# Kernel tuning notes

Hardware: AMD Instinct MI355X
Metric: run time of the kernel (lower is better)

The kernel has to match this reference:

```python
import jax, jax.numpy as jnp
import numpy as np

B, C, N, V, H = 8, 256, 1024, 12, 4
D = C // H  # 64
BN_EPS = 1e-5
NEG = 1e10


def _vconv(x, W, b, g, bt, m4):
    """VointConv block: 1x1 conv + BN(batch stats) + relu, with reset_voint_mask
    applied after every sublayer (as in the torch loop).
    x: [B, Cin, N, V], W: [Cout, Cin], m4: [B, 1, N, V] float mask."""
    y = (jnp.einsum('oc,bcnv->bonv', W, x) + b[None, :, None, None]) * m4
    mu = jnp.mean(y, axis=(0, 2, 3), keepdims=True)
    var = jnp.var(y, axis=(0, 2, 3), keepdims=True)
    y = ((y - mu) * jax.lax.rsqrt(var + BN_EPS) * g[None, :, None, None]
         + bt[None, :, None, None]) * m4
    return jax.nn.relu(y) * m4


def setup_inputs() -> dict:
    key = jax.random.key(0)
    ks = jax.random.split(key, 20)
    inp = {}
    inp['voints_feats'] = jax.random.normal(ks[0], (B, C, N, V), jnp.float32)
    inp['voints_mask'] = (jax.random.uniform(ks[1], (B, N, V)) > 0.3).astype(jnp.float32)
    w = lambda k, shp: (jax.random.normal(k, shp, jnp.float32) * 0.05)
    # embed_layers[0]: VointConv([C, C/heads])
    inp['We'] = w(ks[2], (D, C)); inp['be'] = w(ks[3], (D,))
    inp['ge'] = 1.0 + 0.1 * jax.random.normal(ks[4], (D,), jnp.float32)
    inp['bne'] = 0.1 * jax.random.normal(ks[5], (D,), jnp.float32)
    # embed_atten_layers[0]: VointConv([C/heads, 3*C])
    inp['Wa'] = w(ks[6], (3 * C, D)); inp['ba'] = w(ks[7], (3 * C,))
    inp['ga'] = 1.0 + 0.1 * jax.random.normal(ks[8], (3 * C,), jnp.float32)
    inp['bna'] = 0.1 * jax.random.normal(ks[9], (3 * C,), jnp.float32)
    # to_out[0]: VointConv([C, C])
    inp['Wo'] = w(ks[10], (C, C)); inp['bo'] = w(ks[11], (C,))
    inp['go'] = 1.0 + 0.1 * jax.random.normal(ks[12], (C,), jnp.float32)
    inp['bno'] = 0.1 * jax.random.normal(ks[13], (C,), jnp.float32)
    # feedforward[0]: VointConv([C, C])
    inp['Wf'] = w(ks[14], (C, C)); inp['bf'] = w(ks[15], (C,))
    inp['gf'] = 1.0 + 0.1 * jax.random.normal(ks[16], (C,), jnp.float32)
    inp['bnf'] = 0.1 * jax.random.normal(ks[17], (C,), jnp.float32)
    return inp


def reference(voints_feats, voints_mask, We, be, ge, bne, Wa, ba, ga, bna,
              Wo, bo, go, bno, Wf, bf, gf, bnf):
    mask = voints_mask                      # [B, N, V] float
    m4 = mask[:, None, :, :]                # [B, 1, N, V]
    # embedding to per-head dim, then joint QKV projection
    emb = _vconv(voints_feats, We, be, ge, bne, m4)      # [B, D, N, V]
    qkv = _vconv(emb, Wa, ba, ga, bna, m4)               # [B, 3C, N, V]
    k, q, v = jnp.split(qkv, 3, axis=1)                  # torch.chunk order: k, q, v
    resh = lambda t: t.reshape(B, H, D, N, V)            # 'b (h d) n v -> b h d n v'
    q, k, v = resh(q), resh(k), resh(v)
    scale = float(C) ** (-0.5)
    dots = jnp.einsum('bhdnv,bhdnj->bhnvj', q, k) * scale  # [B,H,N,V,V]
    empty = jnp.sum(mask, axis=-1) == 0                  # [B, N]
    dots = jnp.where(empty[:, None, :, None, None], 0.0, dots)
    # vointsoftmax: bias broadcasts over query dim v (mask[...,None] -> [B,1,N,V,1])
    qbias = jnp.where(mask[:, None, :, :, None] > 0, 0.0, -NEG)
    attn = jax.nn.softmax(dots + qbias, axis=-1) * mask[:, None, :, :, None]
    # faithful to source: 'b h n v j, b h d n v -> b h n v d' (j summed over attn only)
    out = jnp.einsum('bhnvj,bhdnv->bhnvd', attn, v)      # [B,H,N,V,D]
    out = out.transpose(0, 1, 4, 2, 3).reshape(B, C, N, V)  # 'b h n v d -> b (h d) n v'
    out = jnp.where(empty[:, None, :, None], 0.0, out)
    out = _vconv(out, Wo, bo, go, bno, m4)
    x = voints_feats + out
    x = x + _vconv(x, Wf, bf, gf, bnf, m4)
    return x
```

## Files before the change

### kernel.cpp

```cpp
#include <hip/hip_runtime.h>
#include <hip/hip_bf16.h>

typedef __attribute__((ext_vector_type(8))) __bf16 bf16x8;
typedef __attribute__((ext_vector_type(4))) float floatx4;
typedef __attribute__((ext_vector_type(8))) unsigned short ushort8;

namespace {
constexpr int kC  = 256;
constexpr int kNV = 1024 * 12;
constexpr int kP  = 8 * kNV;
constexpr float kEps = 1e-5f;

constexpr size_t OFF_PART   = 2048;
constexpr size_t OFF_WB     = 2048 + 16384;
constexpr size_t OFF_XT     = OFF_WB + 81920;
constexpr size_t OFF_Y1     = OFF_XT + (size_t)kP * 256 / 2;
constexpr size_t OFF_Y2     = OFF_Y1 + (size_t)kP * 64 / 2;
constexpr size_t OFF_Y3     = OFF_Y2 + (size_t)kP * 256 / 2;
}

__device__ __forceinline__ unsigned short f2bf(float f) {
    unsigned int u = __builtin_bit_cast(unsigned int, f);
    u += 0x7FFFu + ((u >> 16) & 1u);
    return (unsigned short)(u >> 16);
}
__device__ __forceinline__ float bf2f(unsigned short h) {
    unsigned int u = ((unsigned int)h) << 16;
    return __builtin_bit_cast(float, u);
}
__device__ __forceinline__ unsigned int f2bf2(float lo, float hi) {
    unsigned int r;
    asm("v_cvt_pk_bf16_f32 %0, %1, %2" : "=v"(r) : "v"(lo), "v"(hi));
    return r;
}

__global__ void convw_kernel(const float* __restrict__ We, const float* __restrict__ Wa,
                             const float* __restrict__ Wo, const float* __restrict__ Wf,
                             unsigned short* __restrict__ dst)
{
    const int f = (blockIdx.x * 256 + threadIdx.x) * 4;
    const float* src; int off, M, K, base;
    if (f < 16384)      { src = We;            off = f;         M = 64;  K = 256; base = 0; }
    else if (f < 32768) { src = Wa + 512 * 64; off = f - 16384; M = 256; K = 64;  base = 16384; }
    else if (f < 98304) { src = Wo;            off = f - 32768; M = 256; K = 256; base = 32768; }
    else                { src = Wf;            off = f - 98304; M = 256; K = 256; base = 98304; }
    const int m = off / K, k = off - m * K;
    const float4 v = *(const float4*)&src[off];
    ushort4 o; o.x = f2bf(v.x); o.y = f2bf(v.y); o.z = f2bf(v.z); o.w = f2bf(v.w);
    *(ushort4*)&dst[base + (k >> 5) * (M * 32) + m * 32 + (k & 31)] = o;
}

__global__ __launch_bounds__(256) void transpose_kernel(
    const float* __restrict__ x, unsigned short* __restrict__ xT)
{
    __shared__ float T[64][65];
    const int p0 = blockIdx.x * 64;
    const int c0 = blockIdx.y * 64;
    const int b  = p0 / kNV;
    const int q0 = p0 - b * kNV;
    const int t  = threadIdx.x;

    const int cl = t >> 2;
    const int pq = (t & 3) * 16;
    const float* src = &x[(size_t)(b * kC + c0 + cl) * kNV + q0 + pq];
    #pragma unroll
    for (int i = 0; i < 4; ++i) {
        const float4 v = *(const float4*)&src[i * 4];
        T[cl][pq + i * 4 + 0] = v.x;
        T[cl][pq + i * 4 + 1] = v.y;
        T[cl][pq + i * 4 + 2] = v.z;
        T[cl][pq + i * 4 + 3] = v.w;
    }
    __syncthreads();
    const int pr = t >> 2;
    const int cb = (t & 3) * 16;
    #pragma unroll
    for (int i = 0; i < 2; ++i) {
        ushort8 o;
        #pragma unroll
        for (int j = 0; j < 8; ++j) o[j] = f2bf(T[cb + i * 8 + j][pr]);
        *(ushort8*)&xT[(size_t)(p0 + pr) * 256 + c0 + cb + i * 8] = o;
    }
}

template<int MODE>
__device__ __forceinline__ ushort8 xform(ushort8 y8, ushort8 x8, float mp,
                                         const float* __restrict__ actA,
                                         const float* __restrict__ actB, int kk)
{
    if constexpr (MODE == 0) {
        return y8;
    } else {
        const float4 a0 = *(const float4*)&actA[kk];
        const float4 a1 = *(const float4*)&actA[kk + 4];
        const float4 b0 = *(const float4*)&actB[kk];
        const float4 b1 = *(const float4*)&actB[kk + 4];
        const float aa[8] = {a0.x, a0.y, a0.z, a0.w, a1.x, a1.y, a1.z, a1.w};
        const float bb[8] = {b0.x, b0.y, b0.z, b0.w, b1.x, b1.y, b1.z, b1.w};
        float v[8];
        #pragma unroll
        for (int j = 0; j < 8; ++j) {
            float t = mp * fmaxf(fmaf(aa[j], bf2f(y8[j]), bb[j]), 0.f);
            if constexpr (MODE == 2) t += bf2f(x8[j]);
            v[j] = t;
        }
        uint4 u;
        u.x = f2bf2(v[0], v[1]); u.y = f2bf2(v[2], v[3]);
        u.z = f2bf2(v[4], v[5]); u.w = f2bf2(v[6], v[7]);
        return __builtin_bit_cast(ushort8, u);
    }
}

template<int BM, int MTOT, int K, int MODE, int SIBS, int MINW>
__global__ __launch_bounds__(256, MINW) void gemm_kernel(
    const unsigned short* __restrict__ Apk, const float* __restrict__ bias,
    const unsigned short* __restrict__ Yprev, const unsigned short* __restrict__ XT,
    const float* __restrict__ mask,
    const float* __restrict__ pPrev, const float* __restrict__ gPrev,
    const float* __restrict__ btPrev,
    unsigned short* __restrict__ Yout, float* __restrict__ partial, int slabsPerBlock)
{
    constexpr int LD = 264;
    constexpr int NT = K / 32;
    constexpr int FM = BM / 64;
    constexpr int FP = 2;
    constexpr int CH = K / 64;
    __shared__ unsigned short Bs[2][32 * LD];
    __shared__ float ActA[256];
    __shared__ float ActB[256];

    const int tid  = threadIdx.x;
    const int w    = tid >> 6, lane = tid & 63, quad = lane >> 4, lt = lane & 15;
    const int mBase = w * 16 * FM;

    int groupId, sib;
    if constexpr (SIBS > 1) {
        const int x = blockIdx.x & 7;
        const int s = blockIdx.x >> 3;
        const int perX = (int)(gridDim.x >> 3) / SIBS;
        sib = s % SIBS;
        groupId = x * perX + s / SIBS;
    } else {
        groupId = blockIdx.x; sib = 0;
    }
    const int chOff = sib * BM;
    const int slab0 = groupId * slabsPerBlock;

    if constexpr (MODE != 0) {
        if (tid < K) {
            float s = 0.f, s2 = 0.f;
            #pragma unroll
            for (int k = 0; k < 8; ++k) {
                s  += pPrev[k * 512 + tid];
                s2 += pPrev[k * 512 + 256 + tid];
            }
            const float mu  = s * (1.f / kP);
            const float var = s2 * (1.f / kP) - mu * mu;
            const float A   = rsqrtf(var + kEps) * gPrev[tid];
            ActA[tid] = A;
            ActB[tid] = fmaf(-mu, A, btPrev[tid]);
        }
        __syncthreads();
    }

    ushort8 Areg[NT][FM];
    #pragma unroll
    for (int t = 0; t < NT; ++t)
        #pragma unroll
        for (int fm = 0; fm < FM; ++fm)
            Areg[t][fm] = *(const ushort8*)&Apk[(size_t)(t * MTOT + chOff + mBase + fm * 16 + lt) * 32 + quad * 8];

    float biR[FM][4];
    #pragma unroll
    for (int fm = 0; fm < FM; ++fm) {
        const float4 b4 = *(const float4*)&bias[chOff + mBase + fm * 16 + quad * 4];
        biR[fm][0] = b4.x; biR[fm][1] = b4.y; biR[fm][2] = b4.z; biR[fm][3] = b4.w;
    }

    float aS[FM][4], aQ[FM][4];
    #pragma unroll
    for (int fm = 0; fm < FM; ++fm)
        #pragma unroll
        for (int i = 0; i < 4; ++i) { aS[fm][i] = 0.f; aQ[fm][i] = 0.f; }

    const int spb = slabsPerBlock;

    {
        const int pBase = slab0 * 32;
        #pragma unroll
        for (int i = 0; i < CH; ++i) {
            const int c = tid + i * 256;
            const int p = c / (K / 8);
            const int kq = (c % (K / 8)) * 8;
            const ushort8 y8 = *(const ushort8*)&Yprev[(size_t)(pBase + p) * K + kq];
            ushort8 o;
            if constexpr (MODE == 0) o = y8;
            else {
                ushort8 x8{};
                if constexpr (MODE == 2) x8 = *(const ushort8*)&XT[(size_t)(pBase + p) * K + kq];
                o = xform<MODE>(y8, x8, mask[pBase + p], ActA, ActB, kq);
            }
            *(ushort8*)&Bs[0][p * LD + kq] = o;
        }
    }
    __syncthreads();

    for (int s = 0; s < spb; ++s) {
        const int pBase = (slab0 + s) * 32;
        const bool hasNext = (s + 1 < spb);

        ushort8 py[CH];
        ushort8 px[(MODE == 2) ? CH : 1];
        if (hasNext) {
            const int pN = (slab0 + s + 1) * 32;
            #pragma unroll
            for (int i = 0; i < CH; ++i) {
                const int c = tid + i * 256;
                const int p = c / (K / 8);
                const int kq = (c % (K / 8)) * 8;
                py[i] = *(const ushort8*)&Yprev[(size_t)(pN + p) * K + kq];
                if constexpr (MODE == 2)
                    px[i] = *(const ushort8*)&XT[(size_t)(pN + p) * K + kq];
            }
        }

        floatx4 acc[FM][FP];
        #pragma unroll
        for (int fm = 0; fm < FM; ++fm)
            #pragma unroll
            for (int fp = 0; fp < FP; ++fp) acc[fm][fp] = (floatx4)0.f;

        const unsigned short* bs = &Bs[s & 1][0];
        #pragma unroll
        for (int t = 0; t < NT; ++t) {
            bf16x8 bF[FP];
            #pragma unroll
            for (int fp = 0; fp < FP; ++fp)
                bF[fp] = *(const bf16x8*)&bs[(fp * 16 + lt) * LD + t * 32 + quad * 8];
            #pragma unroll
            for (int fm = 0; fm < FM; ++fm) {
                const bf16x8 aF = __builtin_bit_cast(bf16x8, Areg[t][fm]);
                #pragma unroll
                for (int fp = 0; fp < FP; ++fp)
                    acc[fm][fp] = __builtin_amdgcn_mfma_f32_16x16x32_bf16(aF, bF[fp], acc[fm][fp], 0, 0, 0);
            }
        }

        float mpv[FP];
        #pragma unroll
        for (int fp = 0; fp < FP; ++fp) mpv[fp] = mask[pBase + fp * 16 + lt];

        #pragma unroll
        for (int fm = 0; fm < FM; ++fm) {
            #pragma unroll
            for (int fp = 0; fp < FP; ++fp) {
                const int pG = pBase + fp * 16 + lt;
                float vv[4];
                #pragma unroll
                for (int i = 0; i < 4; ++i) {
                    const float v = (acc[fm][fp][i] + biR[fm][i]) * mpv[fp];
                    vv[i] = v; aS[fm][i] += v; aQ[fm][i] += v * v;
                }
                uint2 o; o.x = f2bf2(vv[0], vv[1]); o.y = f2bf2(vv[2], vv[3]);
                *(uint2*)&Yout[(size_t)pG * MTOT + chOff + mBase + fm * 16 + quad * 4] = o;
            }
        }

        if (hasNext) {
            const int pN = (slab0 + s + 1) * 32;
            unsigned short* bn = &Bs[(s + 1) & 1][0];
            #pragma unroll
            for (int i = 0; i < CH; ++i) {
                const int c = tid + i * 256;
                const int p = c / (K / 8);
                const int kq = (c % (K / 8)) * 8;
                ushort8 o;
                if constexpr (MODE == 0) o = py[i];
                else {
                    ushort8 x8{};
                    if constexpr (MODE == 2) x8 = px[i];
                    o = xform<MODE>(py[i], x8, mask[pN + p], ActA, ActB, kq);
                }
                *(ushort8*)&bn[p * LD + kq] = o;
            }
        }
        __syncthreads();
    }

    #pragma unroll
    for (int fm = 0; fm < FM; ++fm)
        #pragma unroll
        for (int i = 0; i < 4; ++i) {
            #pragma unroll
            for (int off = 1; off < 16; off <<= 1) {
                aS[fm][i] += __shfl_xor(aS[fm][i], off);
                aQ[fm][i] += __shfl_xor(aQ[fm][i], off);
            }
        }
    if (lt == 0) {
        float* pb = partial + (size_t)(blockIdx.x & 7) * 512;
        #pragma unroll
        for (int fm = 0; fm < FM; ++fm)
            #pragma unroll
            for (int i = 0; i < 4; ++i) {
                const int ch = chOff + mBase + fm * 16 + quad * 4 + i;
                atomicAdd(&pb[ch], aS[fm][i]);
                atomicAdd(&pb[256 + ch], aQ[fm][i]);
            }
    }
}

__global__ __launch_bounds__(256) void final_kernel(
    const unsigned short* __restrict__ xT, const unsigned short* __restrict__ y3,
    const unsigned short* __restrict__ y4,
    const float* __restrict__ p3, const float* __restrict__ g3, const float* __restrict__ bt3,
    const float* __restrict__ p4, const float* __restrict__ g4, const float* __restrict__ bt4,
    const float* __restrict__ mask, float* __restrict__ out)
{
    constexpr int TL = 264;
    __shared__ unsigned short TX[32 * TL];
    __shared__ unsigned short T4[32 * TL];
    __shared__ float PA3[256], PB3[256], PA4[256], PB4[256];
    const int p0 = blockIdx.x * 32;
    const int b  = p0 / kNV;
    const int q0 = p0 - b * kNV;

    {
        const int m = threadIdx.x;
        float s3 = 0.f, q3 = 0.f, s4 = 0.f, q4 = 0.f;
        #pragma unroll
        for (int k = 0; k < 8; ++k) {
            s3 += p3[k * 512 + m]; q3 += p3[k * 512 + 256 + m];
            s4 += p4[k * 512 + m]; q4 += p4[k * 512 + 256 + m];
        }
        const float mu3 = s3 * (1.f / kP);
        const float A3  = rsqrtf(q3 * (1.f / kP) - mu3 * mu3 + kEps) * g3[m];
        PA3[m] = A3; PB3[m] = fmaf(-mu3, A3, bt3[m]);
        const float mu4 = s4 * (1.f / kP);
        const float A4  = rsqrtf(q4 * (1.f / kP) - mu4 * mu4 + kEps) * g4[m];
        PA4[m] = A4; PB4[m] = fmaf(-mu4, A4, bt4[m]);
    }
    __syncthreads();

    #pragma unroll
    for (int i = 0; i < 4; ++i) {
        const int idx = threadIdx.x + i * 256;
        const int p = idx >> 5, c0 = (idx & 31) * 8;
        const ushort8 x8  = *(const ushort8*)&xT[(size_t)(p0 + p) * 256 + c0];
        const ushort8 y38 = *(const ushort8*)&y3[(size_t)(p0 + p) * 256 + c0];
        const ushort8 y48 = *(const ushort8*)&y4[(size_t)(p0 + p) * 256 + c0];
        const float mp = mask[p0 + p];
        ushort8 o;
        #pragma unroll
        for (int j = 0; j < 8; ++j) {
            const int c = c0 + j;
            const float x1 = bf2f(x8[j]) + mp * fmaxf(fmaf(PA3[c], bf2f(y38[j]), PB3[c]), 0.f);
            o[j] = f2bf(x1);
        }
        *(ushort8*)&TX[p * TL + c0] = o;
        *(ushort8*)&T4[p * TL + c0] = y48;
    }
    __syncthreads();

    const int qv = (threadIdx.x & 15) * 2;
    const int cb = threadIdx.x >> 4;
    const float m0v = mask[p0 + qv], m1v = mask[p0 + qv + 1];
    #pragma unroll
    for (int j = 0; j < 16; ++j) {
        const int c = cb + j * 16;
        const float a4 = PA4[c], b4 = PB4[c];
        const size_t ro = (size_t)(b * kC + c) * kNV + q0 + qv;
        float2 o;
        o.x = bf2f(TX[qv * TL + c])       + m0v * fmaxf(fmaf(a4, bf2f(T4[qv * TL + c]), b4), 0.f);
        o.y = bf2f(TX[(qv + 1) * TL + c]) + m1v * fmaxf(fmaf(a4, bf2f(T4[(qv + 1) * TL + c]), b4), 0.f);
        *(float2*)&out[ro] = o;
    }
}

extern "C" void kernel_launch(void* const* d_in, const int* in_sizes, int n_in,
                              void* d_out, int out_size, void* d_ws, size_t ws_size,
                              hipStream_t stream)
{
    const float* x    = (const float*)d_in[0];
    const float* mask = (const float*)d_in[1];
    const float* We   = (const float*)d_in[2];
    const float* be   = (const float*)d_in[3];
    const float* ge   = (const float*)d_in[4];
    const float* bne  = (const float*)d_in[5];
    const float* Wa   = (const float*)d_in[6];
    const float* ba   = (const float*)d_in[7];
    const float* ga   = (const float*)d_in[8];
    const float* bna  = (const float*)d_in[9];
    const float* Wo   = (const float*)d_in[10];
    const float* bo   = (const float*)d_in[11];
    const float* go   = (const float*)d_in[12];
    const float* bno  = (const float*)d_in[13];
    const float* Wf   = (const float*)d_in[14];
    const float* bf   = (const float*)d_in[15];
    const float* gf   = (const float*)d_in[16];
    const float* bnf  = (const float*)d_in[17];
    float* out = (float*)d_out;
    float* ws  = (float*)d_ws;

    float* part = ws + OFF_PART;
    unsigned short* Wb = (unsigned short*)(ws + OFF_WB);
    unsigned short* xT = (unsigned short*)(ws + OFF_XT);
    unsigned short* y1 = (unsigned short*)(ws + OFF_Y1);
    unsigned short* y2 = (unsigned short*)(ws + OFF_Y2);
    unsigned short* y3 = (unsigned short*)(ws + OFF_Y3);

    hipMemsetAsync(part, 0, 16384 * sizeof(float), stream);
    convw_kernel<<<160, 256, 0, stream>>>(We, Wa, Wo, Wf, Wb);
    transpose_kernel<<<dim3(kP / 64, 4), 256, 0, stream>>>(x, xT);

    const dim3 blk(256);

    gemm_kernel<64, 64, 256, 0, 1, 4><<<1024, blk, 0, stream>>>(
        Wb, be, xT, nullptr, mask, nullptr, nullptr, nullptr, y1, part, 3);

    gemm_kernel<128, 256, 64, 1, 2, 4><<<1024, blk, 0, stream>>>(
        Wb + 16384, ba + 512, y1, nullptr, mask, part, ge, bne, y2, part + 4096, 6);

    gemm_kernel<128, 256, 256, 1, 2, 3><<<768, blk, 0, stream>>>(
        Wb + 32768, bo, y2, nullptr, mask, part + 4096, ga + 512, bna + 512, y3, part + 8192, 8);

    gemm_kernel<128, 256, 256, 2, 2, 3><<<768, blk, 0, stream>>>(
        Wb + 98304, bf, y3, xT, mask, part + 8192, go, bno, y2, part + 12288, 8);

    final_kernel<<<kP / 32, blk, 0, stream>>>(
        xT, y3, y2, part + 8192, go, bno, part + 12288, gf, bnf, mask, out);
}
```

Baseline: 389.2 us.

## Triple-buffer GEMM B tiles with two-slab-ahead register prefetch and retune launches

The GEMM main loop moves from double to triple LDS buffering. Global loads of Y, X and the mask are now issued two slabs ahead into alternating register sets, and the LDS store for the next slab happens before the epilogue, with a single lightweight barrier per step. The goal is to hide global memory latency behind the MFMA work. The launch configurations also change: the first GEMM uses fewer, larger blocks, and the two 256x256 GEMMs switch to BM=64 with four sibling blocks and 16 slabs each. In exchange this raises register and LDS pressure, and the loop unrolled by two assumes spb is even.

```diff
diff --git a/kernel.cpp b/kernel.cpp
--- a/kernel.cpp
+++ b/kernel.cpp
@@ -32,6 +32,12 @@
     unsigned int r;
     asm("v_cvt_pk_bf16_f32 %0, %1, %2" : "=v"(r) : "v"(lo), "v"(hi));
     return r;
+}
+
+__device__ __forceinline__ void phase_barrier() {
+    asm volatile("s_waitcnt lgkmcnt(0)" ::: "memory");
+    __builtin_amdgcn_s_barrier();
+    asm volatile("" ::: "memory");
 }
 
 __global__ void convw_kernel(const float* __restrict__ We, const float* __restrict__ Wa,
@@ -120,12 +126,13 @@
     const float* __restrict__ btPrev,
     unsigned short* __restrict__ Yout, float* __restrict__ partial, int slabsPerBlock)
 {
-    constexpr int LD = 264;
+    constexpr int LD = K + 8;
     constexpr int NT = K / 32;
     constexpr int FM = BM / 64;
     constexpr int FP = 2;
     constexpr int CH = K / 64;
-    __shared__ unsigned short Bs[2][32 * LD];
+    constexpr int XH = (MODE == 2) ? CH : 1;
+    __shared__ unsigned short Bs[3][32 * LD];
     __shared__ float ActA[256];
     __shared__ float ActB[256];
 
@@ -144,7 +151,8 @@
         groupId = blockIdx.x; sib = 0;
     }
     const int chOff = sib * BM;
-    const int slab0 = groupId * slabsPerBlock;
+    const int spb   = slabsPerBlock;
+    const int slab0 = groupId * spb;
 
     if constexpr (MODE != 0) {
         if (tid < K) {
@@ -183,7 +191,10 @@
         #pragma unroll
         for (int i = 0; i < 4; ++i) { aS[fm][i] = 0.f; aQ[fm][i] = 0.f; }
 
-    const int spb = slabsPerBlock;
+    ushort8 pyA[CH], pyB[CH];
+    ushort8 pxA[XH], pxB[XH];
+    float   mxA[CH], mxB[CH];
+    float   meA[FP], meB[FP];
 
     {
         const int pBase = slab0 * 32;
@@ -202,25 +213,39 @@
             }
             *(ushort8*)&Bs[0][p * LD + kq] = o;
         }
-    }
-    __syncthreads();
-
-    for (int s = 0; s < spb; ++s) {
-        const int pBase = (slab0 + s) * 32;
-        const bool hasNext = (s + 1 < spb);
-
-        ushort8 py[CH];
-        ushort8 px[(MODE == 2) ? CH : 1];
-        if (hasNext) {
-            const int pN = (slab0 + s + 1) * 32;
+        #pragma unroll
+        for (int fp = 0; fp < FP; ++fp) meA[fp] = mask[pBase + fp * 16 + lt];
+        const int pN = (slab0 + 1) * 32;
+        #pragma unroll
+        for (int i = 0; i < CH; ++i) {
+            const int c = tid + i * 256;
+            const int p = c / (K / 8);
+            const int kq = (c % (K / 8)) * 8;
+            pyA[i] = *(const ushort8*)&Yprev[(size_t)(pN + p) * K + kq];
+            if constexpr (MODE == 2) pxA[i] = *(const ushort8*)&XT[(size_t)(pN + p) * K + kq];
+            if constexpr (MODE != 0) mxA[i] = mask[pN + p];
+        }
+    }
+    phase_barrier();
+
+    auto stepf = [&](int s, int cur,
+                     ushort8 (&uy)[CH], ushort8 (&ux)[XH], float (&umx)[CH], float (&ume)[FP],
+                     ushort8 (&fy)[CH], ushort8 (&fx)[XH], float (&fmx)[CH], float (&fme)[FP]) {
+        if (s + 1 < spb) {
+            const int pE = (slab0 + s + 1) * 32;
+            #pragma unroll
+            for (int fp = 0; fp < FP; ++fp) fme[fp] = mask[pE + fp * 16 + lt];
+        }
+        if (s + 2 < spb) {
+            const int pN = (slab0 + s + 2) * 32;
             #pragma unroll
             for (int i = 0; i < CH; ++i) {
                 const int c = tid + i * 256;
                 const int p = c / (K / 8);
                 const int kq = (c % (K / 8)) * 8;
-                py[i] = *(const ushort8*)&Yprev[(size_t)(pN + p) * K + kq];
-                if constexpr (MODE == 2)
-                    px[i] = *(const ushort8*)&XT[(size_t)(pN + p) * K + kq];
+                fy[i] = *(const ushort8*)&Yprev[(size_t)(pN + p) * K + kq];
+                if constexpr (MODE == 2) fx[i] = *(const ushort8*)&XT[(size_t)(pN + p) * K + kq];
+                if constexpr (MODE != 0) fmx[i] = mask[pN + p];
             }
         }
 
@@ -230,7 +255,7 @@
             #pragma unroll
             for (int fp = 0; fp < FP; ++fp) acc[fm][fp] = (floatx4)0.f;
 
-        const unsigned short* bs = &Bs[s & 1][0];
+        const unsigned short* bs = &Bs[cur][0];
         #pragma unroll
         for (int t = 0; t < NT; ++t) {
             bf16x8 bF[FP];
@@ -246,10 +271,26 @@
             }
         }
 
-        float mpv[FP];
-        #pragma unroll
-        for (int fp = 0; fp < FP; ++fp) mpv[fp] = mask[pBase + fp * 16 + lt];
-
+        if (s + 1 < spb) {
+            const int nb = (cur == 2) ? 0 : cur + 1;
+            unsigned short* bn = &Bs[nb][0];
+            #pragma unroll
+            for (int i = 0; i < CH; ++i) {
+                const int c = tid + i * 256;
+                const int p = c / (K / 8);
+                const int kq = (c % (K / 8)) * 8;
+                ushort8 o;
+                if constexpr (MODE == 0) o = uy[i];
+                else {
+                    ushort8 x8{};
+                    if constexpr (MODE == 2) x8 = ux[i];
+                    o = xform<MODE>(uy[i], x8, umx[i], ActA, ActB, kq);
+                }
+                *(ushort8*)&bn[p * LD + kq] = o;
+            }
+        }
+
+        const int pBase = (slab0 + s) * 32;
         #pragma unroll
         for (int fm = 0; fm < FM; ++fm) {
             #pragma unroll
@@ -258,7 +299,7 @@
                 float vv[4];
                 #pragma unroll
                 for (int i = 0; i < 4; ++i) {
-                    const float v = (acc[fm][fp][i] + biR[fm][i]) * mpv[fp];
+                    const float v = (acc[fm][fp][i] + biR[fm][i]) * ume[fp];
                     vv[i] = v; aS[fm][i] += v; aQ[fm][i] += v * v;
                 }
                 uint2 o; o.x = f2bf2(vv[0], vv[1]); o.y = f2bf2(vv[2], vv[3]);
@@ -266,25 +307,15 @@
             }
         }
 
-        if (hasNext) {
-            const int pN = (slab0 + s + 1) * 32;
-            unsigned short* bn = &Bs[(s + 1) & 1][0];
-            #pragma unroll
-            for (int i = 0; i < CH; ++i) {
-                const int c = tid + i * 256;
-                const int p = c / (K / 8);
-                const int kq = (c % (K / 8)) * 8;
-                ushort8 o;
-                if constexpr (MODE == 0) o = py[i];
-                else {
-                    ushort8 x8{};
-                    if constexpr (MODE == 2) x8 = px[i];
-                    o = xform<MODE>(py[i], x8, mask[pN + p], ActA, ActB, kq);
-                }
-                *(ushort8*)&bn[p * LD + kq] = o;
-            }
-        }
-        __syncthreads();
+        phase_barrier();
+    };
+
+    int cur = 0;
+    for (int s = 0; s < spb; s += 2) {
+        stepf(s,     cur, pyA, pxA, mxA, meA, pyB, pxB, mxB, meB);
+        cur = (cur == 2) ? 0 : cur + 1;
+        stepf(s + 1, cur, pyB, pxB, mxB, meB, pyA, pxA, mxA, meA);
+        cur = (cur == 2) ? 0 : cur + 1;
     }
 
     #pragma unroll
@@ -415,17 +446,17 @@
 
     const dim3 blk(256);
 
-    gemm_kernel<64, 64, 256, 0, 1, 4><<<1024, blk, 0, stream>>>(
-        Wb, be, xT, nullptr, mask, nullptr, nullptr, nullptr, y1, part, 3);
+    gemm_kernel<64, 64, 256, 0, 1, 3><<<768, blk, 0, stream>>>(
+        Wb, be, xT, nullptr, mask, nullptr, nullptr, nullptr, y1, part, 4);
 
     gemm_kernel<128, 256, 64, 1, 2, 4><<<1024, blk, 0, stream>>>(
         Wb + 16384, ba + 512, y1, nullptr, mask, part, ge, bne, y2, part + 4096, 6);
 
-    gemm_kernel<128, 256, 256, 1, 2, 3><<<768, blk, 0, stream>>>(
-        Wb + 32768, bo, y2, nullptr, mask, part + 4096, ga + 512, bna + 512, y3, part + 8192, 8);
-
-    gemm_kernel<128, 256, 256, 2, 2, 3><<<768, blk, 0, stream>>>(
-        Wb + 98304, bf, y3, xT, mask, part + 8192, go, bno, y2, part + 12288, 8);
+    gemm_kernel<64, 256, 256, 1, 4, 3><<<768, blk, 0, stream>>>(
+        Wb + 32768, bo, y2, nullptr, mask, part + 4096, ga + 512, bna + 512, y3, part + 8192, 16);
+
+    gemm_kernel<64, 256, 256, 2, 4, 3><<<768, blk, 0, stream>>>(
+        Wb + 98304, bf, y3, xT, mask, part + 8192, go, bno, y2, part + 12288, 16);
 
     final_kernel<<<kP / 32, blk, 0, stream>>>(
         xT, y3, y2, part + 8192, go, bno, part + 12288, gf, bnf, mask, out);
```

New measurement: 381.0 us. 1.02x faster.

## Restructure GEMM to one 16-channel slice per wave with configurable waves/slab

Applied to the files above, without the earlier changes.

Each wave now owns a single 16-channel M slice instead of FM slices. Block size (NW waves) and slab width (FP*16 points) become template parameters, so the 128-channel GEMMs run 512-thread blocks and the K=64 GEMM uses 64-point slabs. Mask values are prefetched together with the next slab. The epilogue stores and statistics are moved after the next-slab LDS write, and __syncthreads is replaced by a manual lgkmcnt wait plus s_barrier. This is meant to cut per-thread register pressure and raise occupancy and latency hiding, at the cost of more barriers per block and different grid decompositions.

```diff
diff --git a/kernel.cpp b/kernel.cpp
--- a/kernel.cpp
+++ b/kernel.cpp
@@ -32,6 +32,12 @@
     unsigned int r;
     asm("v_cvt_pk_bf16_f32 %0, %1, %2" : "=v"(r) : "v"(lo), "v"(hi));
     return r;
+}
+
+__device__ __forceinline__ void phase_barrier() {
+    asm volatile("s_waitcnt lgkmcnt(0)" ::: "memory");
+    __builtin_amdgcn_s_barrier();
+    asm volatile("" ::: "memory");
 }
 
 __global__ void convw_kernel(const float* __restrict__ We, const float* __restrict__ Wa,
@@ -111,8 +117,8 @@
     }
 }
 
-template<int BM, int MTOT, int K, int MODE, int SIBS, int MINW>
-__global__ __launch_bounds__(256, MINW) void gemm_kernel(
+template<int BM, int MTOT, int K, int MODE, int SIBS, int NW, int FP, int MINW>
+__global__ __launch_bounds__(NW * 64, MINW) void gemm_kernel(
     const unsigned short* __restrict__ Apk, const float* __restrict__ bias,
     const unsigned short* __restrict__ Yprev, const unsigned short* __restrict__ XT,
     const float* __restrict__ mask,
@@ -120,18 +126,21 @@
     const float* __restrict__ btPrev,
     unsigned short* __restrict__ Yout, float* __restrict__ partial, int slabsPerBlock)
 {
-    constexpr int LD = 264;
+    constexpr int THREADS = NW * 64;
+    constexpr int SLAB = FP * 16;
+    constexpr int LD = K + 8;
     constexpr int NT = K / 32;
-    constexpr int FM = BM / 64;
-    constexpr int FP = 2;
-    constexpr int CH = K / 64;
-    __shared__ unsigned short Bs[2][32 * LD];
+    constexpr int KR = K / 8;
+    constexpr int CH = SLAB * KR / THREADS;
+    constexpr int XH = (MODE == 2) ? CH : 1;
+    static_assert(BM == NW * 16, "one 16-channel slice per wave");
+    __shared__ unsigned short Bs[2][SLAB * LD];
     __shared__ float ActA[256];
     __shared__ float ActB[256];
 
     const int tid  = threadIdx.x;
     const int w    = tid >> 6, lane = tid & 63, quad = lane >> 4, lt = lane & 15;
-    const int mBase = w * 16 * FM;
+    const int mBase = w * 16;
 
     int groupId, sib;
     if constexpr (SIBS > 1) {
@@ -144,7 +153,8 @@
         groupId = blockIdx.x; sib = 0;
     }
     const int chOff = sib * BM;
-    const int slab0 = groupId * slabsPerBlock;
+    const int spb   = slabsPerBlock;
+    const int slab0 = groupId * spb;
 
     if constexpr (MODE != 0) {
         if (tid < K) {
@@ -163,35 +173,28 @@
         __syncthreads();
     }
 
-    ushort8 Areg[NT][FM];
+    ushort8 Areg[NT];
     #pragma unroll
     for (int t = 0; t < NT; ++t)
-        #pragma unroll
-        for (int fm = 0; fm < FM; ++fm)
-            Areg[t][fm] = *(const ushort8*)&Apk[(size_t)(t * MTOT + chOff + mBase + fm * 16 + lt) * 32 + quad * 8];
-
-    float biR[FM][4];
-    #pragma unroll
-    for (int fm = 0; fm < FM; ++fm) {
-        const float4 b4 = *(const float4*)&bias[chOff + mBase + fm * 16 + quad * 4];
-        biR[fm][0] = b4.x; biR[fm][1] = b4.y; biR[fm][2] = b4.z; biR[fm][3] = b4.w;
-    }
-
-    float aS[FM][4], aQ[FM][4];
-    #pragma unroll
-    for (int fm = 0; fm < FM; ++fm)
-        #pragma unroll
-        for (int i = 0; i < 4; ++i) { aS[fm][i] = 0.f; aQ[fm][i] = 0.f; }
-
-    const int spb = slabsPerBlock;
-
+        Areg[t] = *(const ushort8*)&Apk[(size_t)(t * MTOT + chOff + mBase + lt) * 32 + quad * 8];
+
+    float biR[4];
     {
-        const int pBase = slab0 * 32;
+        const float4 b4 = *(const float4*)&bias[chOff + mBase + quad * 4];
+        biR[0] = b4.x; biR[1] = b4.y; biR[2] = b4.z; biR[3] = b4.w;
+    }
+
+    float aS[4], aQ[4];
+    #pragma unroll
+    for (int i = 0; i < 4; ++i) { aS[i] = 0.f; aQ[i] = 0.f; }
+
+    {
+        const int pBase = slab0 * SLAB;
         #pragma unroll
         for (int i = 0; i < CH; ++i) {
-            const int c = tid + i * 256;
-            const int p = c / (K / 8);
-            const int kq = (c % (K / 8)) * 8;
+            const int c = tid + i * THREADS;
+            const int p = c / KR;
+            const int kq = (c % KR) * 8;
             const ushort8 y8 = *(const ushort8*)&Yprev[(size_t)(pBase + p) * K + kq];
             ushort8 o;
             if constexpr (MODE == 0) o = y8;
@@ -203,110 +206,103 @@
             *(ushort8*)&Bs[0][p * LD + kq] = o;
         }
     }
-    __syncthreads();
+    float mCur[FP];
+    #pragma unroll
+    for (int fp = 0; fp < FP; ++fp) mCur[fp] = mask[slab0 * SLAB + fp * 16 + lt];
+    phase_barrier();
 
     for (int s = 0; s < spb; ++s) {
-        const int pBase = (slab0 + s) * 32;
+        const int pBase = (slab0 + s) * SLAB;
         const bool hasNext = (s + 1 < spb);
 
         ushort8 py[CH];
-        ushort8 px[(MODE == 2) ? CH : 1];
+        ushort8 px[XH];
+        float mxN[CH];
+        float mNxt[FP];
         if (hasNext) {
-            const int pN = (slab0 + s + 1) * 32;
+            const int pN = pBase + SLAB;
             #pragma unroll
             for (int i = 0; i < CH; ++i) {
-                const int c = tid + i * 256;
-                const int p = c / (K / 8);
-                const int kq = (c % (K / 8)) * 8;
+                const int c = tid + i * THREADS;
+                const int p = c / KR;
+                const int kq = (c % KR) * 8;
                 py[i] = *(const ushort8*)&Yprev[(size_t)(pN + p) * K + kq];
-                if constexpr (MODE == 2)
-                    px[i] = *(const ushort8*)&XT[(size_t)(pN + p) * K + kq];
-            }
-        }
-
-        floatx4 acc[FM][FP];
-        #pragma unroll
-        for (int fm = 0; fm < FM; ++fm)
-            #pragma unroll
-            for (int fp = 0; fp < FP; ++fp) acc[fm][fp] = (floatx4)0.f;
+                if constexpr (MODE == 2) px[i] = *(const ushort8*)&XT[(size_t)(pN + p) * K + kq];
+                if constexpr (MODE != 0) mxN[i] = mask[pN + c / KR];
+            }
+            #pragma unroll
+            for (int fp = 0; fp < FP; ++fp) mNxt[fp] = mask[pN + fp * 16 + lt];
+        }
+
+        floatx4 acc[FP];
+        #pragma unroll
+        for (int fp = 0; fp < FP; ++fp) acc[fp] = (floatx4)0.f;
 
         const unsigned short* bs = &Bs[s & 1][0];
         #pragma unroll
         for (int t = 0; t < NT; ++t) {
-            bf16x8 bF[FP];
-            #pragma unroll
-            for (int fp = 0; fp < FP; ++fp)
-                bF[fp] = *(const bf16x8*)&bs[(fp * 16 + lt) * LD + t * 32 + quad * 8];
-            #pragma unroll
-            for (int fm = 0; fm < FM; ++fm) {
-                const bf16x8 aF = __builtin_bit_cast(bf16x8, Areg[t][fm]);
-                #pragma unroll
-                for (int fp = 0; fp < FP; ++fp)
-                    acc[fm][fp] = __builtin_amdgcn_mfma_f32_16x16x32_bf16(aF, bF[fp], acc[fm][fp], 0, 0, 0);
-            }
-        }
-
-        float mpv[FP];
-        #pragma unroll
-        for (int fp = 0; fp < FP; ++fp) mpv[fp] = mask[pBase + fp * 16 + lt];
-
-        #pragma unroll
-        for (int fm = 0; fm < FM; ++fm) {
+            const bf16x8 aF = __builtin_bit_cast(bf16x8, Areg[t]);
             #pragma unroll
             for (int fp = 0; fp < FP; ++fp) {
-                const int pG = pBase + fp * 16 + lt;
-                float vv[4];
-                #pragma unroll
-                for (int i = 0; i < 4; ++i) {
-                    const float v = (acc[fm][fp][i] + biR[fm][i]) * mpv[fp];
-                    vv[i] = v; aS[fm][i] += v; aQ[fm][i] += v * v;
-                }
-                uint2 o; o.x = f2bf2(vv[0], vv[1]); o.y = f2bf2(vv[2], vv[3]);
-                *(uint2*)&Yout[(size_t)pG * MTOT + chOff + mBase + fm * 16 + quad * 4] = o;
+                const bf16x8 bF = *(const bf16x8*)&bs[(fp * 16 + lt) * LD + t * 32 + quad * 8];
+                acc[fp] = __builtin_amdgcn_mfma_f32_16x16x32_bf16(aF, bF, acc[fp], 0, 0, 0);
             }
         }
 
         if (hasNext) {
-            const int pN = (slab0 + s + 1) * 32;
             unsigned short* bn = &Bs[(s + 1) & 1][0];
             #pragma unroll
             for (int i = 0; i < CH; ++i) {
-                const int c = tid + i * 256;
-                const int p = c / (K / 8);
-                const int kq = (c % (K / 8)) * 8;
+                const int c = tid + i * THREADS;
+                const int p = c / KR;
+                const int kq = (c % KR) * 8;
                 ushort8 o;
                 if constexpr (MODE == 0) o = py[i];
                 else {
                     ushort8 x8{};
                     if constexpr (MODE == 2) x8 = px[i];
-                    o = xform<MODE>(py[i], x8, mask[pN + p], ActA, ActB, kq);
+                    o = xform<MODE>(py[i], x8, mxN[i], ActA, ActB, kq);
                 }
                 *(ushort8*)&bn[p * LD + kq] = o;
             }
         }
-        __syncthreads();
-    }
-
-    #pragma unroll
-    for (int fm = 0; fm < FM; ++fm)
-        #pragma unroll
-        for (int i = 0; i < 4; ++i) {
-            #pragma unroll
-            for (int off = 1; off < 16; off <<= 1) {
-                aS[fm][i] += __shfl_xor(aS[fm][i], off);
-                aQ[fm][i] += __shfl_xor(aQ[fm][i], off);
-            }
-        }
+
+        #pragma unroll
+        for (int fp = 0; fp < FP; ++fp) {
+            const int pG = pBase + fp * 16 + lt;
+            float vv[4];
+            #pragma unroll
+            for (int i = 0; i < 4; ++i) {
+                const float v = (acc[fp][i] + biR[i]) * mCur[fp];
+                vv[i] = v; aS[i] += v; aQ[i] += v * v;
+            }
+            uint2 o; o.x = f2bf2(vv[0], vv[1]); o.y = f2bf2(vv[2], vv[3]);
+            *(uint2*)&Yout[(size_t)pG * MTOT + chOff + mBase + quad * 4] = o;
+        }
+        if (hasNext) {
+            #pragma unroll
+            for (int fp = 0; fp < FP; ++fp) mCur[fp] = mNxt[fp];
+        }
+
+        phase_barrier();
+    }
+
+    #pragma unroll
+    for (int i = 0; i < 4; ++i) {
+        #pragma unroll
+        for (int off = 1; off < 16; off <<= 1) {
+            aS[i] += __shfl_xor(aS[i], off);
+            aQ[i] += __shfl_xor(aQ[i], off);
+        }
+    }
     if (lt == 0) {
         float* pb = partial + (size_t)(blockIdx.x & 7) * 512;
         #pragma unroll
-        for (int fm = 0; fm < FM; ++fm)
-            #pragma unroll
-            for (int i = 0; i < 4; ++i) {
-                const int ch = chOff + mBase + fm * 16 + quad * 4 + i;
-                atomicAdd(&pb[ch], aS[fm][i]);
-                atomicAdd(&pb[256 + ch], aQ[fm][i]);
-            }
+        for (int i = 0; i < 4; ++i) {
+            const int ch = chOff + mBase + quad * 4 + i;
+            atomicAdd(&pb[ch], aS[i]);
+            atomicAdd(&pb[256 + ch], aQ[i]);
+        }
     }
 }
 
@@ -413,20 +409,18 @@
     convw_kernel<<<160, 256, 0, stream>>>(We, Wa, Wo, Wf, Wb);
     transpose_kernel<<<dim3(kP / 64, 4), 256, 0, stream>>>(x, xT);
 
-    const dim3 blk(256);
-
-    gemm_kernel<64, 64, 256, 0, 1, 4><<<1024, blk, 0, stream>>>(
-        Wb, be, xT, nullptr, mask, nullptr, nullptr, nullptr, y1, part, 3);
-
-    gemm_kernel<128, 256, 64, 1, 2, 4><<<1024, blk, 0, stream>>>(
-        Wb + 16384, ba + 512, y1, nullptr, mask, part, ge, bne, y2, part + 4096, 6);
-
-    gemm_kernel<128, 256, 256, 1, 2, 3><<<768, blk, 0, stream>>>(
+    gemm_kernel<64, 64, 256, 0, 1, 4, 2, 3><<<768, 256, 0, stream>>>(
+        Wb, be, xT, nullptr, mask, nullptr, nullptr, nullptr, y1, part, 4);
+
+    gemm_kernel<128, 256, 64, 1, 2, 8, 4, 4><<<768, 512, 0, stream>>>(
+        Wb + 16384, ba + 512, y1, nullptr, mask, part, ge, bne, y2, part + 4096, 4);
+
+    gemm_kernel<128, 256, 256, 1, 2, 8, 2, 4><<<768, 512, 0, stream>>>(
         Wb + 32768, bo, y2, nullptr, mask, part + 4096, ga + 512, bna + 512, y3, part + 8192, 8);
 
-    gemm_kernel<128, 256, 256, 2, 2, 3><<<768, blk, 0, stream>>>(
+    gemm_kernel<128, 256, 256, 2, 2, 8, 2, 4><<<768, 512, 0, stream>>>(
         Wb + 98304, bf, y3, xT, mask, part + 8192, go, bno, y2, part + 12288, 8);
 
-    final_kernel<<<kP / 32, blk, 0, stream>>>(
+    final_kernel<<<kP / 32, 256, 0, stream>>>(
         xT, y3, y2, part + 8192, go, bno, part + 12288, gf, bnf, mask, out);
 }
```

New measurement: 358.7 us. 1.08x faster.
